# Optimization experiments

Measured on AMD Instinct MI355X. Metric: run time of the kernel, lower is better.

## Reference

```python
import jax, jax.numpy as jnp
import numpy as np

B, H, M, TK, NK, D = 4, 8, 1, 512, 511, 512
HD = D // H
NEG_INF = float('-inf')


def setup_inputs() -> dict:
    key = jax.random.key(0)
    ks = jax.random.split(key, 8)
    s = 0.02
    leaves = jax.random.normal(ks[0], (B, M, TK, D), jnp.float32)
    nodes = jax.random.normal(ks[1], (B, M, NK, D), jnp.float32)
    # per-head [left, right] leaf span of each tree node, left <= right
    node_indices = jnp.sort(jax.random.randint(ks[2], (B, H, M, NK, 2), 0, TK), axis=-1)
    key_pad = jnp.zeros((B, M, TK), jnp.bool_)
    node_pad = jnp.zeros((B, M, NK), jnp.bool_)
    Wq = jax.random.normal(ks[3], (D, D), jnp.float32) * s
    Wk = jax.random.normal(ks[4], (D, D), jnp.float32) * s
    Wv = jax.random.normal(ks[5], (D, D), jnp.float32) * s
    Wo = jax.random.normal(ks[6], (D, D), jnp.float32) * s
    bq = jnp.zeros((D,), jnp.float32)
    bk = jnp.zeros((D,), jnp.float32)
    bv = jnp.zeros((D,), jnp.float32)
    bo = jnp.zeros((D,), jnp.float32)
    return dict(leaves=leaves, nodes=nodes, Wq=Wq, Wk=Wk, Wv=Wv, Wo=Wo,
                bq=bq, bk=bk, bv=bv, bo=bo,
                node_indices=node_indices, key_pad=key_pad, node_pad=node_pad)


def _build_masks(node_indices, key_pad, node_pad):
    """Faithful jnp port of WeightMaskEff.build_mask_leaves_subtree."""
    L = M * (TK + NK)
    rg = jnp.arange(TK)
    # --- leaf queries: attend only non-pad leaves (node keys fully masked) ---
    leaf_mask = jnp.concatenate([key_pad, jnp.ones_like(node_pad)], axis=2)
    leaf_mask = leaf_mask.reshape(B, 1, 1, 1, L)                       # (B,1,1,1,L)
    # --- node queries over leaf keys: leaves inside the node's span ---
    idx_q = jnp.swapaxes(node_indices, 2, 3)                           # (B,H,NK,M,2)
    lo = idx_q[..., 0][..., None, None]                                # (B,H,NK,M,1,1)
    hi = idx_q[..., 1][..., None, None]
    leave_npad = (rg < lo) | (rg > hi)                                 # (B,H,NK,M,1,TK)
    leave_npad = leave_npad | jnp.swapaxes(node_pad, 1, 2)[:, None, :, :, None, None]
    leaf_keys_mask = leave_npad | key_pad[:, None, None, None, :, :]   # (B,H,NK,M,M,TK)
    # --- node queries over node keys: span overlap, lower-triangular ---
    in_span = (rg >= node_indices[..., 0:1]) & (rg <= node_indices[..., 1:2])  # (B,H,M,NK,TK)
    nl = in_span.astype(jnp.float32)
    overlap = jnp.tril(jnp.clip(jnp.einsum('bhmit,bhmjt->bhmij', nl, nl), 0.0, 1.0)) > 0
    node_npad = jnp.swapaxes(overlap[:, :, :, :, None, :], 2, 3)       # (B,H,NK,M,1,NK)
    node_keys_mask = (~node_npad) | node_pad[:, None, None, None, :, :]  # (B,H,NK,M,M,NK)
    node_mask = jnp.concatenate([leaf_keys_mask, node_keys_mask], axis=5).reshape(B, H, NK, M, L)
    return leaf_mask, node_mask


def _attention(leaves, nodes, Wq, Wk, Wv, Wo, bq, bk, bv, bo,
               node_indices, key_pad, node_pad):
    TKNK = TK + NK
    L = M * TKNK
    kv_src = jnp.concatenate([leaves, nodes], axis=2)        # (B,M,TKNK,D): key layout [m, tknk]
    q_src = jnp.swapaxes(kv_src, 1, 2).reshape(B, L, D)      # query layout [tknk, m]
    kv = kv_src.reshape(B, L, D)
    q = (q_src @ Wq.T + bq) * (HD ** -0.5)
    k = kv @ Wk.T + bk
    v = kv @ Wv.T + bv
    split = lambda x: jnp.swapaxes(x.reshape(B, L, H, HD), 1, 2)  # (B,H,L,HD)
    qh, kh, vh = split(q), split(k), split(v)
    w = jnp.einsum('bhqd,bhkd->bhqk', qh, kh).reshape(B, H, TKNK, M, L)
    leaf_mask, node_mask = _build_masks(node_indices, key_pad, node_pad)
    w = jnp.concatenate([
        jnp.where(leaf_mask, NEG_INF, w[:, :, :TK]),
        jnp.where(node_mask, NEG_INF, w[:, :, TK:]),
    ], axis=2).reshape(B, H, L, L)
    p = jax.nn.softmax(w, axis=-1)
    out = jnp.einsum('bhqk,bhkd->bhqd', p, vh)
    out = jnp.swapaxes(out, 1, 2).reshape(B, L, D)
    return out @ Wo.T + bo


def reference(leaves, nodes, Wq, Wk, Wv, Wo, bq, bk, bv, bo,
              node_indices, key_pad, node_pad):
    return _attention(leaves, nodes, Wq, Wk, Wv, Wo, bq, bk, bv, bo,
                      node_indices, key_pad, node_pad)
```

## Files before the change

### kernel.cpp

```cpp
#include <hip/hip_runtime.h>
#include <math.h>

#define Bn 4
#define Hn 8
#define TKn 512
#define NKn 511
#define Dn 512
#define HDn 64
#define Ln 1023
#define ROWSn (Bn * Ln)
#define NEG_SENT (-1.0e30f)

typedef __attribute__((ext_vector_type(8))) short short8;
typedef __attribute__((ext_vector_type(4))) short short4v;
typedef __attribute__((ext_vector_type(4))) float f32x4;
typedef unsigned short ushort_t;

__device__ __forceinline__ ushort_t f2bf(float f) {
    union { float f; unsigned int u; } v; v.f = f;
    unsigned int r = v.u + 0x7FFF + ((v.u >> 16) & 1);
    return (ushort_t)(r >> 16);
}
__device__ __forceinline__ unsigned int pk2(float a, float b) {
    return (unsigned int)f2bf(a) | ((unsigned int)f2bf(b) << 16);
}

#define LEAF_U ((Bn * TKn * Dn) / 8)
#define NODE_U ((Bn * NKn * Dn) / 8)
#define W_U    ((Dn * Dn) / 8)
__global__ __launch_bounds__(256) void convert_kernel(
    const float* __restrict__ leaves, const float* __restrict__ nodes,
    const float* __restrict__ Wq, const float* __restrict__ Wk,
    const float* __restrict__ Wv, const float* __restrict__ Wo,
    ushort_t* __restrict__ Xb, ushort_t* __restrict__ Wb,
    ushort_t* __restrict__ Vtz)
{
    int u = blockIdx.x * 256 + threadIdx.x;
    if (u < Bn * Hn * HDn) Vtz[(size_t)u * 1024 + 1023] = 0;
    const float* src;
    ushort_t* dst;
    if (u < LEAF_U) {
        int e = u * 8;
        int b = e / (TKn * Dn);
        int rem = e - b * (TKn * Dn);
        src = leaves + e;
        dst = Xb + (size_t)b * Ln * Dn + rem;
    } else if (u < LEAF_U + NODE_U) {
        int e = (u - LEAF_U) * 8;
        int b = e / (NKn * Dn);
        int rem = e - b * (NKn * Dn);
        src = nodes + e;
        dst = Xb + ((size_t)b * Ln + TKn) * Dn + rem;
    } else {
        int e = u - LEAF_U - NODE_U;
        int w = e / W_U;
        int rem = (e - w * W_U) * 8;
        src = (w == 0 ? Wq : w == 1 ? Wk : w == 2 ? Wv : Wo) + rem;
        dst = Wb + (size_t)w * Dn * Dn + rem;
    }
    float4 f0 = *(const float4*)src;
    float4 f1 = *(const float4*)(src + 4);
    int4 o;
    o.x = (int)pk2(f0.x, f0.y);
    o.y = (int)pk2(f0.z, f0.w);
    o.z = (int)pk2(f1.x, f1.y);
    o.w = (int)pk2(f1.z, f1.w);
    *(int4*)dst = o;
}

__global__ __launch_bounds__(256) void qkv_mfma_kernel(
    const ushort_t* __restrict__ Xb, const ushort_t* __restrict__ Wb,
    const float* __restrict__ bq, const float* __restrict__ bk, const float* __restrict__ bv,
    ushort_t* __restrict__ Qo, ushort_t* __restrict__ Ko, ushort_t* __restrict__ Vt)
{
    const int col0g = blockIdx.y * 64;
    const int which = col0g >> 9;
    const int colm  = col0g & 511;
    const ushort_t* __restrict__ W = Wb + (size_t)which * Dn * Dn;
    const float* __restrict__ bias = (which == 0) ? bq : (which == 1) ? bk : bv;
    const float scale = (which == 0) ? 0.125f : 1.0f;

    __shared__ ushort_t As[128][72];
    __shared__ ushort_t Bs[64][72];

    const int tid = threadIdx.x;
    const int lane = tid & 63, wave = tid >> 6;
    const int ln = lane & 15, quad = lane >> 4;
    const int wm = wave & 1, wn = wave >> 1;
    const int row0 = blockIdx.x * 128;

    const int ar = tid >> 3;
    const int cc = (tid & 7) * 8;
    int arc0 = row0 + ar;        if (arc0 > ROWSn - 1) arc0 = ROWSn - 1;
    int arc1 = row0 + ar + 32;   if (arc1 > ROWSn - 1) arc1 = ROWSn - 1;
    int arc2 = row0 + ar + 64;   if (arc2 > ROWSn - 1) arc2 = ROWSn - 1;
    int arc3 = row0 + ar + 96;   if (arc3 > ROWSn - 1) arc3 = ROWSn - 1;

    f32x4 acc[2][4];
    #pragma unroll
    for (int i = 0; i < 2; ++i)
        #pragma unroll
        for (int j = 0; j < 4; ++j) acc[i][j] = (f32x4){0.f, 0.f, 0.f, 0.f};

    int4 a0 = *(const int4*)&Xb[(size_t)arc0 * Dn + cc];
    int4 a1 = *(const int4*)&Xb[(size_t)arc1 * Dn + cc];
    int4 a2 = *(const int4*)&Xb[(size_t)arc2 * Dn + cc];
    int4 a3 = *(const int4*)&Xb[(size_t)arc3 * Dn + cc];
    int4 b0 = *(const int4*)&W[(size_t)(colm + ar) * Dn + cc];
    int4 b1 = *(const int4*)&W[(size_t)(colm + ar + 32) * Dn + cc];

    for (int k0 = 0; k0 < Dn; k0 += 64) {
        __syncthreads();
        *(int4*)&As[ar][cc]      = a0;
        *(int4*)&As[ar + 32][cc] = a1;
        *(int4*)&As[ar + 64][cc] = a2;
        *(int4*)&As[ar + 96][cc] = a3;
        *(int4*)&Bs[ar][cc]      = b0;
        *(int4*)&Bs[ar + 32][cc] = b1;
        int kn = k0 + 64; if (kn > Dn - 64) kn = Dn - 64;
        a0 = *(const int4*)&Xb[(size_t)arc0 * Dn + kn + cc];
        a1 = *(const int4*)&Xb[(size_t)arc1 * Dn + kn + cc];
        a2 = *(const int4*)&Xb[(size_t)arc2 * Dn + kn + cc];
        a3 = *(const int4*)&Xb[(size_t)arc3 * Dn + kn + cc];
        b0 = *(const int4*)&W[(size_t)(colm + ar) * Dn + kn + cc];
        b1 = *(const int4*)&W[(size_t)(colm + ar + 32) * Dn + kn + cc];
        __syncthreads();

        #pragma unroll
        for (int kc = 0; kc < 2; ++kc) {
            short8 af[2], bf[4];
            #pragma unroll
            for (int ni = 0; ni < 2; ++ni)
                af[ni] = *(const short8*)&Bs[wn * 32 + ni * 16 + ln][kc * 32 + quad * 8];
            #pragma unroll
            for (int mi = 0; mi < 4; ++mi)
                bf[mi] = *(const short8*)&As[wm * 64 + mi * 16 + ln][kc * 32 + quad * 8];
            #pragma unroll
            for (int ni = 0; ni < 2; ++ni)
                #pragma unroll
                for (int mi = 0; mi < 4; ++mi)
                    acc[ni][mi] = __builtin_amdgcn_mfma_f32_16x16x32_bf16(af[ni], bf[mi], acc[ni][mi], 0, 0, 0);
        }
    }

    if (which == 2) {
        const int h = colm >> 6;
        #pragma unroll
        for (int ni = 0; ni < 2; ++ni) {
            const int d0 = wn * 32 + ni * 16 + quad * 4;
            const float4 b4 = *(const float4*)&bias[colm + d0];
            #pragma unroll
            for (int mi = 0; mi < 4; ++mi) {
                int row = row0 + wm * 64 + mi * 16 + ln;
                if (row >= ROWSn) continue;
                int bb = row / Ln;
                int l  = row - bb * Ln;
                size_t vbase = ((size_t)((bb * Hn + h) * HDn + d0)) * 1024 + l;
                Vt[vbase]        = f2bf(acc[ni][mi][0] + b4.x);
                Vt[vbase + 1024] = f2bf(acc[ni][mi][1] + b4.y);
                Vt[vbase + 2048] = f2bf(acc[ni][mi][2] + b4.z);
                Vt[vbase + 3072] = f2bf(acc[ni][mi][3] + b4.w);
            }
        }
    } else {
        ushort_t* __restrict__ Y = (which == 0) ? Qo : Ko;
        #pragma unroll
        for (int ni = 0; ni < 2; ++ni) {
            const int colb = colm + wn * 32 + ni * 16 + quad * 4;
            const float4 b4 = *(const float4*)&bias[colb];
            #pragma unroll
            for (int mi = 0; mi < 4; ++mi) {
                int row = row0 + wm * 64 + mi * 16 + ln;
                if (row >= ROWSn) continue;
                uint2 o;
                o.x = pk2(scale * (acc[ni][mi][0] + b4.x), scale * (acc[ni][mi][1] + b4.y));
                o.y = pk2(scale * (acc[ni][mi][2] + b4.z), scale * (acc[ni][mi][3] + b4.w));
                *(uint2*)&Y[(size_t)row * Dn + colb] = o;
            }
        }
    }
}

__global__ __launch_bounds__(256) void outproj_mfma_kernel(
    const ushort_t* __restrict__ AOb, const ushort_t* __restrict__ Wb,
    const float* __restrict__ bo, float* __restrict__ out)
{
    const ushort_t* __restrict__ W = Wb + (size_t)3 * Dn * Dn;
    __shared__ ushort_t As[64][136];
    __shared__ ushort_t Bs[64][136];

    const int tid = threadIdx.x;
    const int lane = tid & 63, wave = tid >> 6;
    const int ln = lane & 15, quad = lane >> 4;
    const int wm = wave & 1, wn = wave >> 1;
    const int row0 = blockIdx.x * 64;
    const int col0 = blockIdx.y * 64;

    const int ar = tid >> 4;
    const int cc = (tid & 15) * 8;
    int rc0 = row0 + ar;      if (rc0 > ROWSn - 1) rc0 = ROWSn - 1;
    int rc1 = row0 + ar + 16; if (rc1 > ROWSn - 1) rc1 = ROWSn - 1;
    int rc2 = row0 + ar + 32; if (rc2 > ROWSn - 1) rc2 = ROWSn - 1;
    int rc3 = row0 + ar + 48; if (rc3 > ROWSn - 1) rc3 = ROWSn - 1;

    f32x4 acc[2][2];
    #pragma unroll
    for (int i = 0; i < 2; ++i)
        #pragma unroll
        for (int j = 0; j < 2; ++j) acc[i][j] = (f32x4){0.f, 0.f, 0.f, 0.f};

    int4 a0 = *(const int4*)&AOb[(size_t)rc0 * Dn + cc];
    int4 a1 = *(const int4*)&AOb[(size_t)rc1 * Dn + cc];
    int4 a2 = *(const int4*)&AOb[(size_t)rc2 * Dn + cc];
    int4 a3 = *(const int4*)&AOb[(size_t)rc3 * Dn + cc];
    int4 b0 = *(const int4*)&W[(size_t)(col0 + ar) * Dn + cc];
    int4 b1 = *(const int4*)&W[(size_t)(col0 + ar + 16) * Dn + cc];
    int4 b2 = *(const int4*)&W[(size_t)(col0 + ar + 32) * Dn + cc];
    int4 b3 = *(const int4*)&W[(size_t)(col0 + ar + 48) * Dn + cc];

    for (int k0 = 0; k0 < Dn; k0 += 128) {
        __syncthreads();
        *(int4*)&As[ar][cc]      = a0;
        *(int4*)&As[ar + 16][cc] = a1;
        *(int4*)&As[ar + 32][cc] = a2;
        *(int4*)&As[ar + 48][cc] = a3;
        *(int4*)&Bs[ar][cc]      = b0;
        *(int4*)&Bs[ar + 16][cc] = b1;
        *(int4*)&Bs[ar + 32][cc] = b2;
        *(int4*)&Bs[ar + 48][cc] = b3;
        int kn = k0 + 128; if (kn > Dn - 128) kn = Dn - 128;
        a0 = *(const int4*)&AOb[(size_t)rc0 * Dn + kn + cc];
        a1 = *(const int4*)&AOb[(size_t)rc1 * Dn + kn + cc];
        a2 = *(const int4*)&AOb[(size_t)rc2 * Dn + kn + cc];
        a3 = *(const int4*)&AOb[(size_t)rc3 * Dn + kn + cc];
        b0 = *(const int4*)&W[(size_t)(col0 + ar) * Dn + kn + cc];
        b1 = *(const int4*)&W[(size_t)(col0 + ar + 16) * Dn + kn + cc];
        b2 = *(const int4*)&W[(size_t)(col0 + ar + 32) * Dn + kn + cc];
        b3 = *(const int4*)&W[(size_t)(col0 + ar + 48) * Dn + kn + cc];
        __syncthreads();

        #pragma unroll
        for (int kc = 0; kc < 4; ++kc) {
            short8 af[2], bf[2];
            #pragma unroll
            for (int ni = 0; ni < 2; ++ni)
                af[ni] = *(const short8*)&Bs[wn * 32 + ni * 16 + ln][kc * 32 + quad * 8];
            #pragma unroll
            for (int mi = 0; mi < 2; ++mi)
                bf[mi] = *(const short8*)&As[wm * 32 + mi * 16 + ln][kc * 32 + quad * 8];
            #pragma unroll
            for (int ni = 0; ni < 2; ++ni)
                #pragma unroll
                for (int mi = 0; mi < 2; ++mi)
                    acc[ni][mi] = __builtin_amdgcn_mfma_f32_16x16x32_bf16(af[ni], bf[mi], acc[ni][mi], 0, 0, 0);
        }
    }

    #pragma unroll
    for (int ni = 0; ni < 2; ++ni) {
        const int colb = col0 + wn * 32 + ni * 16 + quad * 4;
        const float4 b4 = *(const float4*)&bo[colb];
        #pragma unroll
        for (int mi = 0; mi < 2; ++mi) {
            int row = row0 + wm * 32 + mi * 16 + ln;
            if (row >= ROWSn) continue;
            float4 o;
            o.x = acc[ni][mi][0] + b4.x;
            o.y = acc[ni][mi][1] + b4.y;
            o.z = acc[ni][mi][2] + b4.z;
            o.w = acc[ni][mi][3] + b4.w;
            *(float4*)&out[(size_t)row * Dn + colb] = o;
        }
    }
}

__global__ __launch_bounds__(256) void attn_mfma_kernel(
    const ushort_t* __restrict__ Qb, const ushort_t* __restrict__ Kb,
    const ushort_t* __restrict__ Vt, const int* __restrict__ nodeidx,
    float* __restrict__ Opart, float* __restrict__ mlpart)
{
    const int bid = blockIdx.x;
    const int bh = bid & 31;
    const int qts = 31 - (bid >> 5);
    const int qt = qts >> 1;
    const int sp = qts & 1;
    const int b = bh >> 3, h = bh & 7;
    const int tid = threadIdx.x;
    const int lane = tid & 63, wave = tid >> 6;
    const int ln = lane & 15, quad = lane >> 4;
    const bool leafq = qt < 8;
    const int ktend = leafq ? 8 : (qt + 1);

    __shared__ ushort_t Ks[2][64][72];
    __shared__ ushort_t Vts[2][64][72];
    __shared__ int2 nsp[512];

    const int nbase = (b * Hn + h) * NKn * 2;
    if (!leafq) {
        int i = tid;
        nsp[i] = (i < NKn) ? *(const int2*)&nodeidx[nbase + 2 * i] : (int2){0, -1};
        i = tid + 256;
        nsp[i] = (i < NKn) ? *(const int2*)&nodeidx[nbase + 2 * i] : (int2){0, -1};
    }

    const int q0 = qt * 64 + wave * 16;
    const int rq = q0 + ln;
    const int rqc = (rq < Ln) ? rq : (Ln - 1);
    const ushort_t* qp = Qb + ((size_t)(b * Ln + rqc)) * Dn + h * HDn + quad * 8;
    const short8 qf0 = *(const short8*)qp;
    const short8 qf1 = *(const short8*)(qp + 32);

    const bool qvalid = rq < Ln;
    const int iq = rq - TKn;
    int qlo = 0, qhi = -1;
    if (!leafq && qvalid) {
        int2 t = *(const int2*)&nodeidx[nbase + 2 * iq];
        qlo = t.x; qhi = t.y;
    }

    const ushort_t* Kp = Kb + (size_t)(b * Ln) * Dn + h * HDn;
    const ushort_t* Vp = Vt + (size_t)((b * Hn + h) * HDn) * 1024;

    const int sr = tid >> 3;
    const int cc = (tid & 7) * 8;

    {
        const int k0p = sp * 64;
        int kr0 = k0p + sr;      if (kr0 > Ln - 1) kr0 = Ln - 1;
        int kr1 = k0p + 32 + sr; if (kr1 > Ln - 1) kr1 = Ln - 1;
    }
    int kr0 = sp * 64 + sr;      if (kr0 > Ln - 1) kr0 = Ln - 1;
    int kr1 = sp * 64 + 32 + sr; if (kr1 > Ln - 1) kr1 = Ln - 1;
    int4 ka  = *(const int4*)&Kp[(size_t)kr0 * Dn + cc];
    int4 kb2 = *(const int4*)&Kp[(size_t)kr1 * Dn + cc];
    int4 va  = *(const int4*)&Vp[(size_t)sr * 1024 + sp * 64 + cc];
    int4 vb  = *(const int4*)&Vp[(size_t)(32 + sr) * 1024 + sp * 64 + cc];

    float m_run = NEG_SENT, l_run = 0.f;
    f32x4 O[4];
    #pragma unroll
    for (int nd = 0; nd < 4; ++nd) O[nd] = (f32x4){0.f, 0.f, 0.f, 0.f};

    int cur = 0;
    for (int kt = sp; kt < ktend; kt += 2) {
        const int k0 = kt * 64;

        *(int4*)&Ks[cur][sr][cc]        = ka;
        *(int4*)&Ks[cur][32 + sr][cc]   = kb2;
        *(int4*)&Vts[cur][sr][cc]       = va;
        *(int4*)&Vts[cur][32 + sr][cc]  = vb;

        int ktn = kt + 2; if (ktn > 15) ktn = 15;
        const int kn = ktn * 64;
        int krn0 = kn + sr;      if (krn0 > Ln - 1) krn0 = Ln - 1;
        int krn1 = kn + 32 + sr; if (krn1 > Ln - 1) krn1 = Ln - 1;
        ka  = *(const int4*)&Kp[(size_t)krn0 * Dn + cc];
        kb2 = *(const int4*)&Kp[(size_t)krn1 * Dn + cc];
        va  = *(const int4*)&Vp[(size_t)sr * 1024 + kn + cc];
        vb  = *(const int4*)&Vp[(size_t)(32 + sr) * 1024 + kn + cc];

        __syncthreads();

        f32x4 st[4];
        #pragma unroll
        for (int n = 0; n < 4; ++n) {
            short8 kf0 = *(const short8*)&Ks[cur][n * 16 + ln][quad * 8];
            short8 kf1 = *(const short8*)&Ks[cur][n * 16 + ln][32 + quad * 8];
            f32x4 s = __builtin_amdgcn_mfma_f32_16x16x32_bf16(kf0, qf0,
                        (f32x4){0.f, 0.f, 0.f, 0.f}, 0, 0, 0);
            st[n] = __builtin_amdgcn_mfma_f32_16x16x32_bf16(kf1, qf1, s, 0, 0, 0);
        }

        if (!leafq) {
            if (k0 < TKn) {
                #pragma unroll
                for (int n = 0; n < 4; ++n) {
                    int keyb = k0 + n * 16 + quad * 4;
                    #pragma unroll
                    for (int r = 0; r < 4; ++r) {
                        int key = keyb + r;
                        bool a = (key >= qlo) && (key <= qhi);
                        st[n][r] = a ? st[n][r] : NEG_SENT;
                    }
                }
            } else {
                #pragma unroll
                for (int n = 0; n < 4; ++n) {
                    int idx = k0 + n * 16 + quad * 4 - TKn;
                    int4 sa = *(const int4*)&nsp[idx];
                    int4 sb = *(const int4*)&nsp[idx + 2];
                    bool a0 = (idx + 0 <= iq) && (sa.x <= qhi) && (qlo <= sa.y);
                    bool a1 = (idx + 1 <= iq) && (sa.z <= qhi) && (qlo <= sa.w);
                    bool a2 = (idx + 2 <= iq) && (sb.x <= qhi) && (qlo <= sb.y);
                    bool a3 = (idx + 3 <= iq) && (sb.z <= qhi) && (qlo <= sb.w);
                    st[n][0] = a0 ? st[n][0] : NEG_SENT;
                    st[n][1] = a1 ? st[n][1] : NEG_SENT;
                    st[n][2] = a2 ? st[n][2] : NEG_SENT;
                    st[n][3] = a3 ? st[n][3] : NEG_SENT;
                }
            }
        }

        float mx = NEG_SENT;
        #pragma unroll
        for (int n = 0; n < 4; ++n)
            #pragma unroll
            for (int r = 0; r < 4; ++r) mx = fmaxf(mx, st[n][r]);
        mx = fmaxf(mx, __shfl_xor(mx, 16));
        mx = fmaxf(mx, __shfl_xor(mx, 32));

        float mn = fmaxf(m_run, mx);
        float alpha = __expf(m_run - mn);
        m_run = mn;

        float lsum = 0.f;
        short4v ap[4];
        #pragma unroll
        for (int n = 0; n < 4; ++n) {
            float p[4];
            #pragma unroll
            for (int r = 0; r < 4; ++r) {
                float sv = st[n][r];
                p[r] = (sv == NEG_SENT) ? 0.f : __expf(sv - mn);
                lsum += p[r];
            }
            ap[n] = (short4v){(short)f2bf(p[0]), (short)f2bf(p[1]),
                              (short)f2bf(p[2]), (short)f2bf(p[3])};
        }
        lsum += __shfl_xor(lsum, 16);
        lsum += __shfl_xor(lsum, 32);
        l_run = l_run * alpha + lsum;

        float alr[4];
        #pragma unroll
        for (int r = 0; r < 4; ++r) alr[r] = __shfl(alpha, quad * 4 + r);
        #pragma unroll
        for (int nd = 0; nd < 4; ++nd)
            #pragma unroll
            for (int r = 0; r < 4; ++r) O[nd][r] *= alr[r];

        #pragma unroll
        for (int c = 0; c < 4; ++c) {
            #pragma unroll
            for (int nd = 0; nd < 4; ++nd) {
                short4v bvv = *(const short4v*)&Vts[cur][nd * 16 + ln][c * 16 + quad * 4];
                O[nd] = __builtin_amdgcn_mfma_f32_16x16x16bf16_1k(ap[c], bvv, O[nd], 0, 0, 0);
            }
        }
        cur ^= 1;
    }

    if (quad == 0)
        ((float2*)mlpart)[((sp * 32 + bh) << 10) + q0 + ln] = (float2){m_run, l_run};
    float* obase = Opart + ((size_t)((sp * 32 + bh) << 10)) * 64;
    #pragma unroll
    for (int r = 0; r < 4; ++r) {
        int q = q0 + quad * 4 + r;
        float* orow = obase + (size_t)q * 64;
        #pragma unroll
        for (int nd = 0; nd < 4; ++nd)
            orow[nd * 16 + ln] = O[nd][r];
    }
}

__global__ __launch_bounds__(256) void combine_kernel(
    const float* __restrict__ Opart, const float* __restrict__ mlpart,
    ushort_t* __restrict__ AOb)
{
    const int tid = threadIdx.x;
    const int lane = tid & 63, wave = tid >> 6;
    const int ln = lane & 15, quad = lane >> 4;
    const int w = blockIdx.x * 4 + wave;
    const int row = w * 16 + ln;
    const int bh = row >> 10, q = row & 1023;
    if (q >= Ln) return;

    const float2 ml0 = ((const float2*)mlpart)[(bh << 10) + q];
    const float2 ml1 = ((const float2*)mlpart)[((32 + bh) << 10) + q];
    float M = fmaxf(ml0.x, ml1.x);
    float e0 = __expf(ml0.x - M), e1 = __expf(ml1.x - M);
    float invL = 1.f / (e0 * ml0.y + e1 * ml1.y);
    e0 *= invL; e1 *= invL;

    const float4* O0 = (const float4*)(Opart + ((size_t)(bh << 10) + q) * 64 + quad * 16);
    const float4* O1 = (const float4*)(Opart + ((size_t)((32 + bh) << 10) + q) * 64 + quad * 16);
    unsigned int o[8];
    #pragma unroll
    for (int j = 0; j < 4; ++j) {
        float4 x = O0[j], y = O1[j];
        float r0 = e0 * x.x + e1 * y.x;
        float r1 = e0 * x.y + e1 * y.y;
        float r2 = e0 * x.z + e1 * y.z;
        float r3 = e0 * x.w + e1 * y.w;
        o[2 * j]     = pk2(r0, r1);
        o[2 * j + 1] = pk2(r2, r3);
    }
    ushort_t* dst = AOb + ((size_t)((bh >> 3) * Ln + q)) * Dn + (bh & 7) * HDn + quad * 16;
    *(int4*)dst       = (int4){(int)o[0], (int)o[1], (int)o[2], (int)o[3]};
    *(int4*)(dst + 8) = (int4){(int)o[4], (int)o[5], (int)o[6], (int)o[7]};
}

extern "C" void kernel_launch(void* const* d_in, const int* in_sizes, int n_in,
                              void* d_out, int out_size, void* d_ws, size_t ws_size,
                              hipStream_t stream)
{
    const float* leaves = (const float*)d_in[0];
    const float* nodes  = (const float*)d_in[1];
    const float* Wq = (const float*)d_in[2];
    const float* Wk = (const float*)d_in[3];
    const float* Wv = (const float*)d_in[4];
    const float* Wo = (const float*)d_in[5];
    const float* bq = (const float*)d_in[6];
    const float* bk = (const float*)d_in[7];
    const float* bv = (const float*)d_in[8];
    const float* bo = (const float*)d_in[9];
    const int* nodeidx = (const int*)d_in[10];

    ushort_t* ws = (ushort_t*)d_ws;
    const size_t N = (size_t)ROWSn * Dn;
    ushort_t* Xb  = ws;
    ushort_t* Wb  = Xb + N;
    ushort_t* Qb  = Wb + (size_t)4 * Dn * Dn;
    ushort_t* Kb  = Qb + N;
    ushort_t* Vt  = Kb + N;
    ushort_t* AOb = Vt + (size_t)Bn * Hn * HDn * 1024;
    float* Opart  = (float*)(AOb + N);
    float* mlpart = Opart + (size_t)2 * 32 * 1024 * 64;

    convert_kernel<<<1535, 256, 0, stream>>>(leaves, nodes, Wq, Wk, Wv, Wo, Xb, Wb, Vt);

    dim3 pgrid(32, 24);
    qkv_mfma_kernel<<<pgrid, 256, 0, stream>>>(Xb, Wb, bq, bk, bv, Qb, Kb, Vt);

    attn_mfma_kernel<<<1024, 256, 0, stream>>>(Qb, Kb, Vt, nodeidx, Opart, mlpart);

    combine_kernel<<<512, 256, 0, stream>>>(Opart, mlpart, AOb);

    dim3 ogrid(64, 8);
    outproj_mfma_kernel<<<ogrid, 256, 0, stream>>>(AOb, Wb, bo, (float*)d_out);
}
```

Before: 132.1 us.

## Widen QKV GEMM tile to 128 columns and double-buffer LDS

The QKV projection kernel now computes 128x128 output tiles per block instead of 128x64, halving the grid and reusing each loaded A tile across twice as many columns. Shared memory is double-buffered so one barrier per k-step suffices instead of two. The V-transpose epilogue now computes the head index per column fragment because a tile spans two heads. This raises accumulator registers and LDS use per block, which may lower occupancy, and the smaller grid (384 blocks) may underfill the GPU. Dead code in the attention kernel is also removed.

```diff
diff --git a/kernel.cpp b/kernel.cpp
--- a/kernel.cpp
+++ b/kernel.cpp
@@ -73,15 +73,15 @@
     const float* __restrict__ bq, const float* __restrict__ bk, const float* __restrict__ bv,
     ushort_t* __restrict__ Qo, ushort_t* __restrict__ Ko, ushort_t* __restrict__ Vt)
 {
-    const int col0g = blockIdx.y * 64;
+    const int col0g = blockIdx.y * 128;
     const int which = col0g >> 9;
     const int colm  = col0g & 511;
     const ushort_t* __restrict__ W = Wb + (size_t)which * Dn * Dn;
     const float* __restrict__ bias = (which == 0) ? bq : (which == 1) ? bk : bv;
     const float scale = (which == 0) ? 0.125f : 1.0f;
 
-    __shared__ ushort_t As[128][72];
-    __shared__ ushort_t Bs[64][72];
+    __shared__ ushort_t As[2][128][72];
+    __shared__ ushort_t Bs[2][128][72];
 
     const int tid = threadIdx.x;
     const int lane = tid & 63, wave = tid >> 6;
@@ -96,9 +96,9 @@
     int arc2 = row0 + ar + 64;   if (arc2 > ROWSn - 1) arc2 = ROWSn - 1;
     int arc3 = row0 + ar + 96;   if (arc3 > ROWSn - 1) arc3 = ROWSn - 1;
 
-    f32x4 acc[2][4];
+    f32x4 acc[4][4];
     #pragma unroll
-    for (int i = 0; i < 2; ++i)
+    for (int i = 0; i < 4; ++i)
         #pragma unroll
         for (int j = 0; j < 4; ++j) acc[i][j] = (f32x4){0.f, 0.f, 0.f, 0.f};
 
@@ -108,15 +108,19 @@
     int4 a3 = *(const int4*)&Xb[(size_t)arc3 * Dn + cc];
     int4 b0 = *(const int4*)&W[(size_t)(colm + ar) * Dn + cc];
     int4 b1 = *(const int4*)&W[(size_t)(colm + ar + 32) * Dn + cc];
-
+    int4 b2 = *(const int4*)&W[(size_t)(colm + ar + 64) * Dn + cc];
+    int4 b3 = *(const int4*)&W[(size_t)(colm + ar + 96) * Dn + cc];
+
+    int cur = 0;
     for (int k0 = 0; k0 < Dn; k0 += 64) {
-        __syncthreads();
-        *(int4*)&As[ar][cc]      = a0;
-        *(int4*)&As[ar + 32][cc] = a1;
-        *(int4*)&As[ar + 64][cc] = a2;
-        *(int4*)&As[ar + 96][cc] = a3;
-        *(int4*)&Bs[ar][cc]      = b0;
-        *(int4*)&Bs[ar + 32][cc] = b1;
+        *(int4*)&As[cur][ar][cc]      = a0;
+        *(int4*)&As[cur][ar + 32][cc] = a1;
+        *(int4*)&As[cur][ar + 64][cc] = a2;
+        *(int4*)&As[cur][ar + 96][cc] = a3;
+        *(int4*)&Bs[cur][ar][cc]      = b0;
+        *(int4*)&Bs[cur][ar + 32][cc] = b1;
+        *(int4*)&Bs[cur][ar + 64][cc] = b2;
+        *(int4*)&Bs[cur][ar + 96][cc] = b3;
         int kn = k0 + 64; if (kn > Dn - 64) kn = Dn - 64;
         a0 = *(const int4*)&Xb[(size_t)arc0 * Dn + kn + cc];
         a1 = *(const int4*)&Xb[(size_t)arc1 * Dn + kn + cc];
@@ -124,31 +128,35 @@
         a3 = *(const int4*)&Xb[(size_t)arc3 * Dn + kn + cc];
         b0 = *(const int4*)&W[(size_t)(colm + ar) * Dn + kn + cc];
         b1 = *(const int4*)&W[(size_t)(colm + ar + 32) * Dn + kn + cc];
+        b2 = *(const int4*)&W[(size_t)(colm + ar + 64) * Dn + kn + cc];
+        b3 = *(const int4*)&W[(size_t)(colm + ar + 96) * Dn + kn + cc];
         __syncthreads();
 
         #pragma unroll
         for (int kc = 0; kc < 2; ++kc) {
-            short8 af[2], bf[4];
-            #pragma unroll
-            for (int ni = 0; ni < 2; ++ni)
-                af[ni] = *(const short8*)&Bs[wn * 32 + ni * 16 + ln][kc * 32 + quad * 8];
+            short8 af[4], bf[4];
+            #pragma unroll
+            for (int ni = 0; ni < 4; ++ni)
+                af[ni] = *(const short8*)&Bs[cur][wn * 64 + ni * 16 + ln][kc * 32 + quad * 8];
             #pragma unroll
             for (int mi = 0; mi < 4; ++mi)
-                bf[mi] = *(const short8*)&As[wm * 64 + mi * 16 + ln][kc * 32 + quad * 8];
-            #pragma unroll
-            for (int ni = 0; ni < 2; ++ni)
+                bf[mi] = *(const short8*)&As[cur][wm * 64 + mi * 16 + ln][kc * 32 + quad * 8];
+            #pragma unroll
+            for (int ni = 0; ni < 4; ++ni)
                 #pragma unroll
                 for (int mi = 0; mi < 4; ++mi)
                     acc[ni][mi] = __builtin_amdgcn_mfma_f32_16x16x32_bf16(af[ni], bf[mi], acc[ni][mi], 0, 0, 0);
         }
+        cur ^= 1;
     }
 
     if (which == 2) {
-        const int h = colm >> 6;
-        #pragma unroll
-        for (int ni = 0; ni < 2; ++ni) {
-            const int d0 = wn * 32 + ni * 16 + quad * 4;
-            const float4 b4 = *(const float4*)&bias[colm + d0];
+        #pragma unroll
+        for (int ni = 0; ni < 4; ++ni) {
+            const int colb = colm + wn * 64 + ni * 16 + quad * 4;
+            const int h = colb >> 6;
+            const int d0 = colb & 63;
+            const float4 b4 = *(const float4*)&bias[colb];
             #pragma unroll
             for (int mi = 0; mi < 4; ++mi) {
                 int row = row0 + wm * 64 + mi * 16 + ln;
@@ -165,8 +173,8 @@
     } else {
         ushort_t* __restrict__ Y = (which == 0) ? Qo : Ko;
         #pragma unroll
-        for (int ni = 0; ni < 2; ++ni) {
-            const int colb = colm + wn * 32 + ni * 16 + quad * 4;
+        for (int ni = 0; ni < 4; ++ni) {
+            const int colb = colm + wn * 64 + ni * 16 + quad * 4;
             const float4 b4 = *(const float4*)&bias[colb];
             #pragma unroll
             for (int mi = 0; mi < 4; ++mi) {
@@ -324,11 +332,6 @@
     const int sr = tid >> 3;
     const int cc = (tid & 7) * 8;
 
-    {
-        const int k0p = sp * 64;
-        int kr0 = k0p + sr;      if (kr0 > Ln - 1) kr0 = Ln - 1;
-        int kr1 = k0p + 32 + sr; if (kr1 > Ln - 1) kr1 = Ln - 1;
-    }
     int kr0 = sp * 64 + sr;      if (kr0 > Ln - 1) kr0 = Ln - 1;
     int kr1 = sp * 64 + 32 + sr; if (kr1 > Ln - 1) kr1 = Ln - 1;
     int4 ka  = *(const int4*)&Kp[(size_t)kr0 * Dn + cc];
@@ -529,7 +532,7 @@
 
     convert_kernel<<<1535, 256, 0, stream>>>(leaves, nodes, Wq, Wk, Wv, Wo, Xb, Wb, Vt);
 
-    dim3 pgrid(32, 24);
+    dim3 pgrid(32, 12);
     qkv_mfma_kernel<<<pgrid, 256, 0, stream>>>(Xb, Wb, bq, bk, bv, Qb, Kb, Vt);
 
     attn_mfma_kernel<<<1024, 256, 0, stream>>>(Qb, Kb, Vt, nodeidx, Opart, mlpart);
```

Result: no change. 132.9 us (+0.6%).
